# Performance work log

Hardware: AMD Instinct MI355X
Metric: run time of the kernel (lower is better)

The kernel has to match this reference:

```python
import jax, jax.numpy as jnp
import numpy as np
from jax import lax

DN = ('NHWC', 'HWIO', 'NHWC')
N_MEM = 2000  # memory slots
BN_EPS = 1e-3


def _conv(x, w, b):
    # tf.nn.conv2d stride 2, SAME, NHWC / HWIO
    return lax.conv_general_dilated(x, w, (2, 2), 'SAME', dimension_numbers=DN) + b


def _convt(x, w, b):
    # tf.nn.conv2d_transpose; w is TF layout [kh, kw, out_ch, in_ch]
    return lax.conv_transpose(x, w, (2, 2), 'SAME', dimension_numbers=DN,
                              transpose_kernel=True) + b


def _bn(x, g, b):
    # BatchNormalization(training=True): batch statistics over N,H,W
    m = jnp.mean(x, axis=(0, 1, 2))
    v = jnp.var(x, axis=(0, 1, 2))
    return g * (x - m) * lax.rsqrt(v + BN_EPS) + b


def setup_inputs() -> dict:
    key = jax.random.key(0)
    ks = iter(jax.random.split(key, 40))
    def gn(shape, s=0.05):
        return jax.random.normal(next(ks), shape, jnp.float32) * s
    inp = {'x': jax.random.uniform(next(ks), (16, 256, 256, 3), jnp.float32)}
    inp.update(
        w_e1=gn((1, 1, 3, 16)), b_e1=gn((16,)),
        g_bn1=jnp.ones(16, jnp.float32), be_bn1=jnp.zeros(16, jnp.float32),
        w_e2=gn((3, 3, 16, 32)), b_e2=gn((32,)),
        g_bn2=jnp.ones(32, jnp.float32), be_bn2=jnp.zeros(32, jnp.float32),
        w_e3=gn((3, 3, 32, 64)), b_e3=gn((64,)),
        g_bn3=jnp.ones(64, jnp.float32), be_bn3=jnp.zeros(64, jnp.float32),
        w_mem=gn((1, 1, N_MEM, 64)),
        w_d1=gn((3, 3, 32, 64)), b_d1=gn((32,)),
        g_bnt1=jnp.ones(32, jnp.float32), be_bnt1=jnp.zeros(32, jnp.float32),
        w_d2=gn((3, 3, 16, 32)), b_d2=gn((16,)),
        g_bnt2=jnp.ones(16, jnp.float32), be_bnt2=jnp.zeros(16, jnp.float32),
        w_d3=gn((3, 3, 3, 16)), b_d3=gn((3,)),
    )
    return inp


def reference(x, w_e1, b_e1, g_bn1, be_bn1, w_e2, b_e2, g_bn2, be_bn2,
              w_e3, b_e3, g_bn3, be_bn3, w_mem,
              w_d1, b_d1, g_bnt1, be_bnt1, w_d2, b_d2, g_bnt2, be_bnt2,
              w_d3, b_d3):
    # ---- encode ----
    h = jax.nn.relu(_bn(_conv(x, w_e1, b_e1), g_bn1, be_bn1))   # [B,128,128,16]
    h = jax.nn.relu(_bn(_conv(h, w_e2, b_e2), g_bn2, be_bn2))   # [B,64,64,32]
    z = jax.nn.relu(_bn(_conv(h, w_e3, b_e3), g_bn3, be_bn3))   # [B,32,32,64]
    # ---- memory addressing ----
    mem = w_mem[0, 0]                                            # [N, 64]
    num = jnp.einsum('bhwc,nc->bhwn', z, mem)
    den = jnp.einsum('bhwc,nc->bhwn', z * z, mem * mem)
    att = jax.nn.softmax((num + 1e-12) / (den + 1e-12), axis=-1)  # [B,32,32,N]
    d = att - 1.0 / N_MEM                                        # hard shrinkage
    renorm = jnp.clip(jax.nn.relu(d) * att / (jnp.abs(d) + 1e-12),
                      1e-12, 1.0 - 1e-12)
    z_hat = jnp.einsum('bhwn,nc->bhwc', renorm, mem)             # [B,32,32,64]
    # ---- decode ----
    t = jax.nn.relu(_bn(_convt(z_hat, w_d1, b_d1), g_bnt1, be_bnt1))  # [B,64,64,32]
    t = jax.nn.relu(_bn(_convt(t, w_d2, b_d2), g_bnt2, be_bnt2))      # [B,128,128,16]
    x_hat = jnp.clip(_convt(t, w_d3, b_d3), 1e-12, 1.0 - 1e-12)       # [B,256,256,3]
    return x_hat
```

## Files before the change

kernel.cpp:

```cpp
#include <hip/hip_runtime.h>
#include <math.h>

typedef __bf16 bf16x8 __attribute__((ext_vector_type(8)));
typedef __bf16 bf16x4 __attribute__((ext_vector_type(4)));
typedef float  f32x16 __attribute__((ext_vector_type(16)));

static __device__ __forceinline__ f32x16 zero16() {
  f32x16 v;
  #pragma unroll
  for (int i = 0; i < 16; ++i) v[i] = 0.f;
  return v;
}
static __device__ __forceinline__ unsigned int bfbits(__bf16 b) {
  return (unsigned int)__builtin_bit_cast(unsigned short, b);
}
static __device__ __forceinline__ bf16x8 mk8(unsigned int a, unsigned int b,
                                             unsigned int c, unsigned int d) {
  uint4 t; t.x = a; t.y = b; t.z = c; t.w = d;
  return __builtin_bit_cast(bf16x8, t);
}

__global__ __launch_bounds__(256) void k_conv1(const float* __restrict__ x,
    const float* __restrict__ w, const float* __restrict__ b, float* __restrict__ y,
    float* __restrict__ partials) {
  int t = blockIdx.x*256 + threadIdx.x;
  int ox = t & 127, oy = (t >> 7) & 127, bb = t >> 14;
  const float* xp = x + ((size_t)((bb*256 + 2*oy)*256 + 2*ox))*3;
  float x0 = xp[0], x1 = xp[1], x2 = xp[2];
  float4 rg[4];
  float4* yp = (float4*)(y + (size_t)t*16);
  #pragma unroll
  for (int g = 0; g < 4; ++g) {
    float4 r;
    r.x = b[g*4+0] + x0*w[g*4+0] + x1*w[16+g*4+0] + x2*w[32+g*4+0];
    r.y = b[g*4+1] + x0*w[g*4+1] + x1*w[16+g*4+1] + x2*w[32+g*4+1];
    r.z = b[g*4+2] + x0*w[g*4+2] + x1*w[16+g*4+2] + x2*w[32+g*4+2];
    r.w = b[g*4+3] + x0*w[g*4+3] + x1*w[16+g*4+3] + x2*w[32+g*4+3];
    rg[g] = r;
    yp[g] = r;
  }
  float4 s4[4], q4[4];
  #pragma unroll
  for (int g=0; g<4; ++g) {
    s4[g] = rg[g];
    q4[g] = make_float4(rg[g].x*rg[g].x, rg[g].y*rg[g].y, rg[g].z*rg[g].z, rg[g].w*rg[g].w);
  }
  #pragma unroll
  for (int off=1; off<64; off<<=1) {
    #pragma unroll
    for (int g=0; g<4; ++g) {
      s4[g].x += __shfl_xor(s4[g].x, off); s4[g].y += __shfl_xor(s4[g].y, off);
      s4[g].z += __shfl_xor(s4[g].z, off); s4[g].w += __shfl_xor(s4[g].w, off);
      q4[g].x += __shfl_xor(q4[g].x, off); q4[g].y += __shfl_xor(q4[g].y, off);
      q4[g].z += __shfl_xor(q4[g].z, off); q4[g].w += __shfl_xor(q4[g].w, off);
    }
  }
  __shared__ float red[4][32];
  int wv = threadIdx.x >> 6, lane = threadIdx.x & 63;
  if (lane == 0) {
    #pragma unroll
    for (int g=0; g<4; ++g) {
      *(float4*)&red[wv][g*4]      = s4[g];
      *(float4*)&red[wv][16 + g*4] = q4[g];
    }
  }
  __syncthreads();
  if (threadIdx.x < 32)
    partials[(size_t)blockIdx.x*32 + threadIdx.x] =
      red[0][threadIdx.x]+red[1][threadIdx.x]+red[2][threadIdx.x]+red[3][threadIdx.x];
}

template<int C,int CSPLIT>
__global__ __launch_bounds__(256) void k_finalize2(const float* __restrict__ partials, int nblk,
    double inv_n, const float* __restrict__ g, const float* __restrict__ be, float* __restrict__ ss) {
  const int COUTT = C/CSPLIT;
  const int NSTAT = 2*C;
  const int PER = 256/NSTAT;
  __shared__ double red[256];
  int tid = threadIdx.x;
  int st = tid % NSTAT, sub = tid / NSTAT;
  int c = st % C, kind = st / C;
  int cq = c / COUTT, j = c % COUTT;
  int nb = nblk / CSPLIT;
  double acc = 0.0;
  #pragma unroll 4
  for (int i = sub; i < nb; i += PER) {
    int bq = cq + i*CSPLIT;
    acc += (double)partials[(size_t)bq*2*COUTT + kind*COUTT + j];
  }
  red[tid] = acc;
  __syncthreads();
  for (int off = PER>>1; off > 0; off >>= 1) {
    if (sub < off) red[tid] += red[tid + off*NSTAT];
    __syncthreads();
  }
  if (tid < C) {
    double mean = red[tid]*inv_n;
    double var  = red[C+tid]*inv_n - mean*mean;
    float scale = g[tid] * rsqrtf((float)var + 1e-3f);
    float shift = be[tid] - (float)mean*scale;
    ss[tid] = scale; ss[C+tid] = shift;
  }
}

template<int CIN,int COUT,int CSPLIT,int HIN,int HOUT,bool BN>
__global__ __launch_bounds__(256) void k_conv_bn(const float* __restrict__ in,
    const float* __restrict__ w, const float* __restrict__ bias,
    const float* __restrict__ ss, float* __restrict__ y, float* __restrict__ partials) {
  const int COUTT = COUT/CSPLIT;
  const int NW4 = COUTT/4;
  __shared__ float4 wlds[9*CIN*NW4];
  int bid = blockIdx.x;
  int cq  = bid % CSPLIT;
  int pxb = bid / CSPLIT;
  int c0  = cq*COUTT;
  for (int e = threadIdx.x; e < 9*CIN*NW4; e += 256) {
    int r = e / NW4, cg = e % NW4;
    wlds[e] = *(const float4*)(w + (size_t)r*COUT + c0 + cg*4);
  }
  __syncthreads();
  int t0 = pxb*256 + threadIdx.x;
  float4 acc[NW4];
  #pragma unroll
  for (int g=0; g<NW4; ++g) acc[g] = *(const float4*)(bias + c0 + g*4);
  int ox = t0 % HOUT, oy = (t0/HOUT) % HOUT, bb = t0/(HOUT*HOUT);
  #pragma unroll 1
  for (int dy=0; dy<3; ++dy) {
    #pragma unroll 1
    for (int dx=0; dx<3; ++dx) {
      int tap = dy*3+dx;
      int iy = 2*oy + dy, ix = 2*ox + dx;
      if (iy < HIN && ix < HIN) {
        const float* bp = in + ((size_t)(bb*HIN + iy)*HIN + ix)*CIN;
        #pragma unroll
        for (int ci4=0; ci4<CIN/4; ++ci4) {
          float4 v = *(const float4*)(bp + ci4*4);
          if (BN) {
            float4 sc = *(const float4*)(ss + ci4*4);
            float4 sh = *(const float4*)(ss + CIN + ci4*4);
            v.x = fmaxf(0.f, fmaf(v.x, sc.x, sh.x));
            v.y = fmaxf(0.f, fmaf(v.y, sc.y, sh.y));
            v.z = fmaxf(0.f, fmaf(v.z, sc.z, sh.z));
            v.w = fmaxf(0.f, fmaf(v.w, sc.w, sh.w));
          }
          float va[4] = {v.x, v.y, v.z, v.w};
          #pragma unroll
          for (int k=0;k<4;++k) {
            float vk = va[k];
            #pragma unroll
            for (int g=0; g<NW4; ++g) {
              float4 w4 = wlds[(tap*CIN + ci4*4 + k)*NW4 + g];
              acc[g].x = fmaf(vk, w4.x, acc[g].x);
              acc[g].y = fmaf(vk, w4.y, acc[g].y);
              acc[g].z = fmaf(vk, w4.z, acc[g].z);
              acc[g].w = fmaf(vk, w4.w, acc[g].w);
            }
          }
        }
      }
    }
  }
  float4* yp = (float4*)(y + (size_t)t0*COUT + c0);
  #pragma unroll
  for (int g=0;g<NW4;++g) yp[g] = acc[g];
  float4 s4[NW4], q4[NW4];
  #pragma unroll
  for (int g=0; g<NW4; ++g) {
    s4[g] = acc[g];
    q4[g] = make_float4(acc[g].x*acc[g].x, acc[g].y*acc[g].y,
                        acc[g].z*acc[g].z, acc[g].w*acc[g].w);
  }
  #pragma unroll
  for (int off=1; off<64; off<<=1) {
    #pragma unroll
    for (int g=0; g<NW4; ++g) {
      s4[g].x += __shfl_xor(s4[g].x, off); s4[g].y += __shfl_xor(s4[g].y, off);
      s4[g].z += __shfl_xor(s4[g].z, off); s4[g].w += __shfl_xor(s4[g].w, off);
      q4[g].x += __shfl_xor(q4[g].x, off); q4[g].y += __shfl_xor(q4[g].y, off);
      q4[g].z += __shfl_xor(q4[g].z, off); q4[g].w += __shfl_xor(q4[g].w, off);
    }
  }
  __shared__ float red[4][2*COUTT];
  int wv = threadIdx.x >> 6, lane = threadIdx.x & 63;
  if (lane == 0) {
    #pragma unroll
    for (int g=0; g<NW4; ++g) {
      *(float4*)&red[wv][g*4]         = s4[g];
      *(float4*)&red[wv][COUTT + g*4] = q4[g];
    }
  }
  __syncthreads();
  if (threadIdx.x < 2*COUTT)
    partials[(size_t)bid*2*COUTT + threadIdx.x] =
      red[0][threadIdx.x]+red[1][threadIdx.x]+red[2][threadIdx.x]+red[3][threadIdx.x];
}


__global__ __launch_bounds__(256) void k_prep_z(const float* __restrict__ y3,
    const float* __restrict__ ss,
    __bf16* __restrict__ ZH, __bf16* __restrict__ ZL,
    __bf16* __restrict__ Z2H, __bf16* __restrict__ Z2L) {
  int t = blockIdx.x*256 + threadIdx.x;
  float4 v = ((const float4*)y3)[t];
  int c0 = (t*4) & 63;
  float4 sc = *(const float4*)(ss + c0);
  float4 sh = *(const float4*)(ss + 64 + c0);
  float vv[4];
  vv[0] = fmaxf(0.f, fmaf(v.x, sc.x, sh.x));
  vv[1] = fmaxf(0.f, fmaf(v.y, sc.y, sh.y));
  vv[2] = fmaxf(0.f, fmaf(v.z, sc.z, sh.z));
  vv[3] = fmaxf(0.f, fmaf(v.w, sc.w, sh.w));
  bf16x4 h, l, h2, l2;
  #pragma unroll
  for (int i=0;i<4;++i) {
    float f = vv[i];
    __bf16 hb = (__bf16)f;
    h[i] = hb; l[i] = (__bf16)(f - (float)hb);
    float q = f*f;
    __bf16 qb = (__bf16)q;
    h2[i] = qb; l2[i] = (__bf16)(q - (float)qb);
  }
  ((bf16x4*)ZH)[t] = h;  ((bf16x4*)ZL)[t] = l;
  ((bf16x4*)Z2H)[t] = h2; ((bf16x4*)Z2L)[t] = l2;
}

__global__ __launch_bounds__(256) void k_prep_m(const float* __restrict__ mem,
    __bf16* __restrict__ MH, __bf16* __restrict__ ML,
    __bf16* __restrict__ M2H, __bf16* __restrict__ M2L,
    __bf16* __restrict__ MHT, __bf16* __restrict__ MLT) {
  int t = blockIdx.x*256 + threadIdx.x;
  int n = t >> 4, c0 = (t & 15)*4;
  float4 v = make_float4(0.f,0.f,0.f,0.f);
  if (n < 2000) v = *(const float4*)(mem + (size_t)n*64 + c0);
  float vv[4] = {v.x, v.y, v.z, v.w};
  bf16x4 h, l, h2, l2;
  #pragma unroll
  for (int i=0;i<4;++i) {
    float f = vv[i];
    __bf16 hb = (__bf16)f;
    h[i] = hb; l[i] = (__bf16)(f - (float)hb);
    float q = f*f;
    __bf16 qb = (__bf16)q;
    h2[i] = qb; l2[i] = (__bf16)(q - (float)qb);
  }
  *(bf16x4*)(MH  + (size_t)n*64 + c0) = h;
  *(bf16x4*)(ML  + (size_t)n*64 + c0) = l;
  *(bf16x4*)(M2H + (size_t)n*64 + c0) = h2;
  *(bf16x4*)(M2L + (size_t)n*64 + c0) = l2;
  #pragma unroll
  for (int i=0;i<4;++i) {
    MHT[(size_t)(c0+i)*2048 + n] = h[i];
    MLT[(size_t)(c0+i)*2048 + n] = l[i];
  }
}

__global__ __launch_bounds__(256) void k_pass1(
    const __bf16* __restrict__ ZH, const __bf16* __restrict__ ZL,
    const __bf16* __restrict__ Z2H, const __bf16* __restrict__ Z2L,
    const __bf16* __restrict__ MH, const __bf16* __restrict__ ML,
    const __bf16* __restrict__ M2H, const __bf16* __restrict__ M2L,
    float* __restrict__ partM, float* __restrict__ partS) {
  int pb = blockIdx.x & 127, chunk = blockIdx.x >> 7;
  int wave = threadIdx.x >> 6, lane = threadIdx.x & 63;
  int p0 = pb*128 + wave*32;
  int col = lane & 31, hi = lane >> 5;
  bf16x8 bzh[4], bzl[4], b2h[4], b2l[4];
  size_t zoff = (size_t)(p0 + col)*64 + hi*8;
  #pragma unroll
  for (int ks=0;ks<4;++ks) {
    bzh[ks] = *(const bf16x8*)(ZH  + zoff + ks*16);
    bzl[ks] = *(const bf16x8*)(ZL  + zoff + ks*16);
    b2h[ks] = *(const bf16x8*)(Z2H + zoff + ks*16);
    b2l[ks] = *(const bf16x8*)(Z2L + zoff + ks*16);
  }
  float m = -3.4e38f, S = 0.f;
  int nbase = chunk*256;
  #pragma unroll 2
  for (int t=0; t<8; ++t) {
    int n0 = nbase + t*32;
    size_t arow = (size_t)(n0 + col)*64 + hi*8;
    f32x16 num = zero16(), den = zero16();
    #pragma unroll
    for (int ks=0;ks<4;++ks) {
      bf16x8 amh = *(const bf16x8*)(MH + arow + ks*16);
      bf16x8 aml = *(const bf16x8*)(ML + arow + ks*16);
      num = __builtin_amdgcn_mfma_f32_32x32x16_bf16(amh, bzh[ks], num, 0,0,0);
      num = __builtin_amdgcn_mfma_f32_32x32x16_bf16(amh, bzl[ks], num, 0,0,0);
      num = __builtin_amdgcn_mfma_f32_32x32x16_bf16(aml, bzh[ks], num, 0,0,0);
      bf16x8 a2h = *(const bf16x8*)(M2H + arow + ks*16);
      bf16x8 a2l = *(const bf16x8*)(M2L + arow + ks*16);
      den = __builtin_amdgcn_mfma_f32_32x32x16_bf16(a2h, b2h[ks], den, 0,0,0);
      den = __builtin_amdgcn_mfma_f32_32x32x16_bf16(a2h, b2l[ks], den, 0,0,0);
      den = __builtin_amdgcn_mfma_f32_32x32x16_bf16(a2l, b2h[ks], den, 0,0,0);
    }
    bool maskt = (n0 + 32 > 2000);
    float sv[16];
    float tmax = -3.4e38f;
    #pragma unroll
    for (int r=0;r<16;++r) {
      float s = (num[r] + 1e-12f) * __builtin_amdgcn_rcpf(den[r] + 1e-12f);
      if (maskt) {
        int nn = n0 + (r&3) + 8*(r>>2) + 4*hi;
        if (nn >= 2000) s = -3.4e38f;
      }
      sv[r] = s;
      tmax = fmaxf(tmax, s);
    }
    float mn = fmaxf(m, tmax);
    float ssum = 0.f;
    #pragma unroll
    for (int r=0;r<16;++r) ssum += __expf(sv[r] - mn);
    S = S*__expf(m - mn) + ssum;
    m = mn;
  }
  float mo = __shfl_xor(m, 32);
  float So = __shfl_xor(S, 32);
  float mf = fmaxf(m, mo);
  float Sf = S*__expf(m - mf) + So*__expf(mo - mf);
  if (lane < 32) {
    int p = p0 + col;
    partM[chunk*16384 + p] = mf;
    partS[chunk*16384 + p] = Sf;
  }
}

__global__ __launch_bounds__(256) void k_pass2(
    const __bf16* __restrict__ ZH, const __bf16* __restrict__ ZL,
    const __bf16* __restrict__ Z2H, const __bf16* __restrict__ Z2L,
    const __bf16* __restrict__ MH, const __bf16* __restrict__ ML,
    const __bf16* __restrict__ M2H, const __bf16* __restrict__ M2L,
    const __bf16* __restrict__ MHT, const __bf16* __restrict__ MLT,
    const float* __restrict__ partM, const float* __restrict__ partS,
    float* __restrict__ ZP) {
  int pb = blockIdx.x & 127, chunk = blockIdx.x >> 7;
  int wave = threadIdx.x >> 6, lane = threadIdx.x & 63;
  int p0 = pb*128 + wave*32;
  int col = lane & 31, hi = lane >> 5;
  bf16x8 bzh[4], bzl[4], b2h[4], b2l[4];
  size_t zoff = (size_t)(p0 + col)*64 + hi*8;
  #pragma unroll
  for (int ks=0;ks<4;++ks) {
    bzh[ks] = *(const bf16x8*)(ZH  + zoff + ks*16);
    bzl[ks] = *(const bf16x8*)(ZL  + zoff + ks*16);
    b2h[ks] = *(const bf16x8*)(Z2H + zoff + ks*16);
    b2l[ks] = *(const bf16x8*)(Z2L + zoff + ks*16);
  }
  int p = p0 + col;
  float pmv[8];
  float Mp = -3.4e38f;
  #pragma unroll
  for (int c=0;c<8;++c) { pmv[c] = partM[c*16384 + p]; Mp = fmaxf(Mp, pmv[c]); }
  float Ssum = 0.f;
  #pragma unroll
  for (int c=0;c<8;++c) Ssum += partS[c*16384 + p] * __expf(pmv[c] - Mp);
  float CM  = Mp + __logf(Ssum);
  float thr = CM - 7.6009025f;
  f32x16 za0 = zero16(), za1 = zero16();
  int nbase = chunk*256;
  #pragma unroll 2
  for (int t=0; t<8; ++t) {
    int n0 = nbase + t*32;
    size_t arow = (size_t)(n0 + col)*64 + hi*8;
    f32x16 num = zero16(), den = zero16();
    #pragma unroll
    for (int ks=0;ks<4;++ks) {
      bf16x8 amh = *(const bf16x8*)(MH + arow + ks*16);
      bf16x8 aml = *(const bf16x8*)(ML + arow + ks*16);
      num = __builtin_amdgcn_mfma_f32_32x32x16_bf16(amh, bzh[ks], num, 0,0,0);
      num = __builtin_amdgcn_mfma_f32_32x32x16_bf16(amh, bzl[ks], num, 0,0,0);
      num = __builtin_amdgcn_mfma_f32_32x32x16_bf16(aml, bzh[ks], num, 0,0,0);
      bf16x8 a2h = *(const bf16x8*)(M2H + arow + ks*16);
      bf16x8 a2l = *(const bf16x8*)(M2L + arow + ks*16);
      den = __builtin_amdgcn_mfma_f32_32x32x16_bf16(a2h, b2h[ks], den, 0,0,0);
      den = __builtin_amdgcn_mfma_f32_32x32x16_bf16(a2h, b2l[ks], den, 0,0,0);
      den = __builtin_amdgcn_mfma_f32_32x32x16_bf16(a2l, b2h[ks], den, 0,0,0);
    }
    bool maskt = (n0 + 32 > 2000);
    float rv[16];
    #pragma unroll
    for (int r=0;r<16;++r) {
      float s = (num[r] + 1e-12f) * __builtin_amdgcn_rcpf(den[r] + 1e-12f);
      float att = __expf(s - CM);
      float rr = (s > thr) ? att : 0.f;
      if (maskt) {
        int nn = n0 + (r&3) + 8*(r>>2) + 4*hi;
        if (nn >= 2000) rr = 0.f;
      }
      rv[r] = rr;
    }
    unsigned int qh[8];
    #pragma unroll
    for (int qd=0; qd<4; ++qd) {
      #pragma unroll
      for (int pr=0; pr<2; ++pr) {
        float r0 = rv[qd*4 + pr*2], r1 = rv[qd*4 + pr*2 + 1];
        qh[qd*2+pr] = bfbits((__bf16)r0) | (bfbits((__bf16)r1) << 16);
      }
    }
    unsigned int qhp[8];
    #pragma unroll
    for (int i=0;i<8;++i) qhp[i] = (unsigned int)__shfl_xor((int)qh[i], 32);
    bf16x8 f1h = hi ? mk8(qhp[2],qhp[3],qh[2],qh[3]) : mk8(qh[0],qh[1],qhp[0],qhp[1]);
    bf16x8 f2h = hi ? mk8(qhp[6],qhp[7],qh[6],qh[7]) : mk8(qh[4],qh[5],qhp[4],qhp[5]);
    #pragma unroll
    for (int kh=0; kh<2; ++kh) {
      bf16x8 fh = kh ? f2h : f1h;
      size_t bofs = (size_t)col*2048 + n0 + kh*16 + hi*8;
      bf16x8 bmh0 = *(const bf16x8*)(MHT + bofs);
      bf16x8 bml0 = *(const bf16x8*)(MLT + bofs);
      bf16x8 bmh1 = *(const bf16x8*)(MHT + bofs + (size_t)32*2048);
      bf16x8 bml1 = *(const bf16x8*)(MLT + bofs + (size_t)32*2048);
      za0 = __builtin_amdgcn_mfma_f32_32x32x16_bf16(fh, bmh0, za0, 0,0,0);
      za0 = __builtin_amdgcn_mfma_f32_32x32x16_bf16(fh, bml0, za0, 0,0,0);
      za1 = __builtin_amdgcn_mfma_f32_32x32x16_bf16(fh, bmh1, za1, 0,0,0);
      za1 = __builtin_amdgcn_mfma_f32_32x32x16_bf16(fh, bml1, za1, 0,0,0);
    }
  }
  size_t base = (size_t)chunk << 20;
  #pragma unroll
  for (int r=0;r<16;++r) {
    int prow = (r&3) + 8*(r>>2) + 4*hi;
    size_t o = base + (size_t)(p0 + prow)*64 + col;
    ZP[o]      = za0[r];
    ZP[o + 32] = za1[r];
  }
}

__global__ __launch_bounds__(256) void k_zcomb(const float* __restrict__ ZP,
                                               float* __restrict__ Gz) {
  int t = blockIdx.x*256 + threadIdx.x;
  float a = 0.f;
  #pragma unroll
  for (int c=0;c<8;++c) a += ZP[(size_t)c*1048576 + t];
  Gz[t] = a;
}

template<int CIN,int COUT,int CSPLIT,int HIN,bool BN>
__global__ __launch_bounds__(256) void k_convt_bn(const float* __restrict__ in,
    const float* __restrict__ w, const float* __restrict__ bias,
    const float* __restrict__ ss, float* __restrict__ y, float* __restrict__ partials) {
  const int COUTT = COUT/CSPLIT;
  const int HOUT = 2*HIN;
  __shared__ float4 wlds[4*COUTT*(CIN/4)];
  int bid = blockIdx.x;
  int cq = bid % CSPLIT; int rest = bid / CSPLIT;
  int cls = rest % 4;    int pxb = rest / 4;
  int pm = cls >> 1, pn = cls & 1;
  int c0 = cq*COUTT;
  int NTI = (pm == 0) ? 2 : 1;
  int NTJ = (pn == 0) ? 2 : 1;
  int NT = NTI*NTJ;
  for (int e = threadIdx.x; e < NT*COUTT*(CIN/4); e += 256) {
    int tl = e / (COUTT*(CIN/4));
    int rem = e % (COUTT*(CIN/4));
    int cc = rem / (CIN/4), ci4 = rem % (CIN/4);
    int ki = pm + 2*(tl / NTJ), kj = pn + 2*(tl % NTJ);
    wlds[e] = *(const float4*)(w + ((size_t)(ki*3+kj)*COUT + c0 + cc)*CIN + ci4*4);
  }
  __syncthreads();
  int t0 = pxb*256 + threadIdx.x;
  float acc[COUTT];
  #pragma unroll
  for (int cc=0;cc<COUTT;++cc) acc[cc] = bias[c0+cc];
  int nx = t0 % HIN, my = (t0/HIN) % HIN, bb = t0/(HIN*HIN);
  #pragma unroll 1
  for (int ti=0; ti<NTI; ++ti) {
    #pragma unroll 1
    for (int tj=0; tj<NTJ; ++tj) {
      int tl = ti*NTJ + tj;
      int i = my - ti, j = nx - tj;
      if (i >= 0 && j >= 0) {
        const float* bp = in + ((size_t)(bb*HIN + i)*HIN + j)*CIN;
        #pragma unroll
        for (int ci4=0; ci4<CIN/4; ++ci4) {
          float4 v = *(const float4*)(bp + ci4*4);
          if (BN) {
            float4 sc = *(const float4*)(ss + ci4*4);
            float4 sh = *(const float4*)(ss + CIN + ci4*4);
            v.x = fmaxf(0.f, fmaf(v.x, sc.x, sh.x));
            v.y = fmaxf(0.f, fmaf(v.y, sc.y, sh.y));
            v.z = fmaxf(0.f, fmaf(v.z, sc.z, sh.z));
            v.w = fmaxf(0.f, fmaf(v.w, sc.w, sh.w));
          }
          #pragma unroll
          for (int cc=0;cc<COUTT;++cc) {
            float4 w4 = wlds[(tl*COUTT + cc)*(CIN/4) + ci4];
            float a = acc[cc];
            a = fmaf(v.x, w4.x, a);
            a = fmaf(v.y, w4.y, a);
            a = fmaf(v.z, w4.z, a);
            a = fmaf(v.w, w4.w, a);
            acc[cc] = a;
          }
        }
      }
    }
  }
  int m = 2*my + pm, n = 2*nx + pn;
  float* yp = y + ((size_t)(bb*HOUT + m)*HOUT + n)*COUT + c0;
  #pragma unroll
  for (int g=0;g<COUTT/4;++g)
    ((float4*)yp)[g] = make_float4(acc[g*4], acc[g*4+1], acc[g*4+2], acc[g*4+3]);
  float s[COUTT], q[COUTT];
  #pragma unroll
  for (int cc=0;cc<COUTT;++cc) { s[cc] = acc[cc]; q[cc] = acc[cc]*acc[cc]; }
  #pragma unroll
  for (int off=1; off<64; off<<=1) {
    #pragma unroll
    for (int cc=0;cc<COUTT;++cc) {
      s[cc] += __shfl_xor(s[cc], off);
      q[cc] += __shfl_xor(q[cc], off);
    }
  }
  __shared__ float red[4][2*COUTT];
  int wv = threadIdx.x >> 6, lane = threadIdx.x & 63;
  if (lane == 0) {
    #pragma unroll
    for (int cc=0;cc<COUTT;++cc) { red[wv][cc] = s[cc]; red[wv][COUTT+cc] = q[cc]; }
  }
  __syncthreads();
  if (threadIdx.x < 2*COUTT)
    partials[(size_t)bid*2*COUTT + threadIdx.x] =
      red[0][threadIdx.x]+red[1][threadIdx.x]+red[2][threadIdx.x]+red[3][threadIdx.x];
}

__global__ __launch_bounds__(256) void k_convt_final(const float* __restrict__ in,
    const float* __restrict__ w, const float* __restrict__ bias,
    const float* __restrict__ ss, float* __restrict__ out) {
  const int CIN=16, HIN=128, HOUT=256;
  __shared__ float4 wlds[4*3*4];
  int cls = blockIdx.x & 3;
  int pxb = blockIdx.x >> 2;
  int pm = cls >> 1, pn = cls & 1;
  int NTI = (pm == 0) ? 2 : 1;
  int NTJ = (pn == 0) ? 2 : 1;
  int NT = NTI*NTJ;
  if (threadIdx.x < NT*3*4) {
    int e = threadIdx.x;
    int tl = e / 12, rem = e % 12;
    int c = rem / 4, ci4 = rem % 4;
    int ki = pm + 2*(tl / NTJ), kj = pn + 2*(tl % NTJ);
    wlds[e] = *(const float4*)(w + ((size_t)(ki*3+kj)*3 + c)*CIN + ci4*4);
  }
  __syncthreads();
  int t = pxb*256 + threadIdx.x;
  int nx = t % HIN, my = (t/HIN) % HIN, bb = t/(HIN*HIN);
  float a0 = bias[0], a1 = bias[1], a2 = bias[2];
  #pragma unroll 1
  for (int ti=0; ti<NTI; ++ti) {
    #pragma unroll 1
    for (int tj=0; tj<NTJ; ++tj) {
      int tl = ti*NTJ + tj;
      int i = my - ti, j = nx - tj;
      if (i >= 0 && j >= 0) {
        const float* bp = in + ((size_t)(bb*HIN + i)*HIN + j)*CIN;
        #pragma unroll
        for (int ci4=0; ci4<4; ++ci4) {
          float4 v = *(const float4*)(bp + ci4*4);
          float4 sc = *(const float4*)(ss + ci4*4);
          float4 sh = *(const float4*)(ss + CIN + ci4*4);
          v.x = fmaxf(0.f, fmaf(v.x, sc.x, sh.x));
          v.y = fmaxf(0.f, fmaf(v.y, sc.y, sh.y));
          v.z = fmaxf(0.f, fmaf(v.z, sc.z, sh.z));
          v.w = fmaxf(0.f, fmaf(v.w, sc.w, sh.w));
          float4 w0 = wlds[(tl*3 + 0)*4 + ci4];
          float4 w1 = wlds[(tl*3 + 1)*4 + ci4];
          float4 w2 = wlds[(tl*3 + 2)*4 + ci4];
          a0 = fmaf(v.x, w0.x, a0); a0 = fmaf(v.y, w0.y, a0);
          a0 = fmaf(v.z, w0.z, a0); a0 = fmaf(v.w, w0.w, a0);
          a1 = fmaf(v.x, w1.x, a1); a1 = fmaf(v.y, w1.y, a1);
          a1 = fmaf(v.z, w1.z, a1); a1 = fmaf(v.w, w1.w, a1);
          a2 = fmaf(v.x, w2.x, a2); a2 = fmaf(v.y, w2.y, a2);
          a2 = fmaf(v.z, w2.z, a2); a2 = fmaf(v.w, w2.w, a2);
        }
      }
    }
  }
  int m = 2*my + pm, n = 2*nx + pn;
  float* op = out + ((size_t)(bb*HOUT + m)*HOUT + n)*3;
  op[0] = fminf(fmaxf(a0, 1e-12f), 1.0f);
  op[1] = fminf(fmaxf(a1, 1e-12f), 1.0f);
  op[2] = fminf(fmaxf(a2, 1e-12f), 1.0f);
}

extern "C" void kernel_launch(void* const* d_in, const int* in_sizes, int n_in,
                              void* d_out, int out_size, void* d_ws, size_t ws_size,
                              hipStream_t stream) {
  const float* x    = (const float*)d_in[0];
  const float* w_e1 = (const float*)d_in[1];
  const float* b_e1 = (const float*)d_in[2];
  const float* g1   = (const float*)d_in[3];
  const float* be1  = (const float*)d_in[4];
  const float* w_e2 = (const float*)d_in[5];
  const float* b_e2 = (const float*)d_in[6];
  const float* g2   = (const float*)d_in[7];
  const float* be2  = (const float*)d_in[8];
  const float* w_e3 = (const float*)d_in[9];
  const float* b_e3 = (const float*)d_in[10];
  const float* g3   = (const float*)d_in[11];
  const float* be3  = (const float*)d_in[12];
  const float* wmem = (const float*)d_in[13];
  const float* w_d1 = (const float*)d_in[14];
  const float* b_d1 = (const float*)d_in[15];
  const float* gt1  = (const float*)d_in[16];
  const float* bet1 = (const float*)d_in[17];
  const float* w_d2 = (const float*)d_in[18];
  const float* b_d2 = (const float*)d_in[19];
  const float* gt2  = (const float*)d_in[20];
  const float* bet2 = (const float*)d_in[21];
  const float* w_d3 = (const float*)d_in[22];
  const float* b_d3 = (const float*)d_in[23];
  float* out = (float*)d_out;

  float* ws = (float*)d_ws;
  float* A  = ws;
  float* Cc = A  + 4194304;
  float* E  = Cc + 2097152;
  float* Gz = E  + 1048576;
  float* ZP = Gz + 1048576;
  float* bfbase = ZP + 8388608;
  __bf16* ZH  = (__bf16*)bfbase;
  __bf16* ZL  = ZH  + 16384*64;
  __bf16* Z2H = ZL  + 16384*64;
  __bf16* Z2L = Z2H + 16384*64;
  __bf16* MH  = Z2L + 16384*64;
  __bf16* ML  = MH  + 2048*64;
  __bf16* M2H = ML  + 2048*64;
  __bf16* M2L = M2H + 2048*64;
  __bf16* MHT = M2L + 2048*64;
  __bf16* MLT = MHT + 64*2048;
  float* PT   = (float*)(MLT + 64*2048);
  float* SS   = PT + 131072;
  float* PM   = SS + 256;
  float* PS   = PM + 131072;
  (void)ws_size; (void)in_sizes; (void)n_in; (void)out_size;

  k_conv1<<<1024,256,0,stream>>>(x, w_e1, b_e1, A, PT);
  k_finalize2<16,1><<<1,256,0,stream>>>(PT, 1024, 1.0/262144.0, g1, be1, SS);
  k_conv_bn<16,32,2,128,64,true><<<512,256,0,stream>>>(A, w_e2, b_e2, SS, Cc, PT);
  k_finalize2<32,2><<<1,256,0,stream>>>(PT, 512, 1.0/65536.0, g2, be2, SS);
  k_conv_bn<32,64,8,64,32,true><<<512,256,0,stream>>>(Cc, w_e3, b_e3, SS, E, PT);
  k_finalize2<64,8><<<1,256,0,stream>>>(PT, 512, 1.0/16384.0, g3, be3, SS);
  k_prep_m<<<128,256,0,stream>>>(wmem, MH, ML, M2H, M2L, MHT, MLT);
  k_prep_z<<<1024,256,0,stream>>>(E, SS, ZH, ZL, Z2H, Z2L);
  k_pass1<<<1024,256,0,stream>>>(ZH, ZL, Z2H, Z2L, MH, ML, M2H, M2L, PM, PS);
  k_pass2<<<1024,256,0,stream>>>(ZH, ZL, Z2H, Z2L, MH, ML, M2H, M2L, MHT, MLT, PM, PS, ZP);
  k_zcomb<<<4096,256,0,stream>>>(ZP, Gz);
  k_convt_bn<64,32,2,32,false><<<512,256,0,stream>>>(Gz, w_d1, b_d1, nullptr, Cc, PT);
  k_finalize2<32,2><<<1,256,0,stream>>>(PT, 512, 1.0/65536.0, gt1, bet1, SS);
  k_convt_bn<32,16,1,64,true><<<1024,256,0,stream>>>(Cc, w_d2, b_d2, SS, A, PT);
  k_finalize2<16,1><<<1,256,0,stream>>>(PT, 1024, 1.0/262144.0, gt2, bet2, SS);
  k_convt_final<<<4096,256,0,stream>>>(A, w_d3, b_d3, SS, out);
}
```

Baseline: 400.9 us.

## Switch memory-attention passes to 16x16x32 MFMA tiles with smaller per-wave blocks

Rewrites both memory-addressing passes to use 16x16x32 bf16 MFMA instead of 32x32x16. Each wave now handles 16 positions instead of 32, and the grid doubles to 2048 blocks. The softmax max/sum reduction now runs over four lane groups, and pass2 rebuilds the A fragment for the second GEMM with lane shuffles. Occupancy hints are added to the launch bounds. The intent is fewer accumulator registers and higher occupancy for better latency hiding, at the cost of more memory-row reloads per position and more shuffle work.

Result: slower. 582.7 us (+45.4%).

```diff
diff --git a/kernel.cpp b/kernel.cpp
--- a/kernel.cpp
+++ b/kernel.cpp
@@ -3,12 +3,10 @@
 
 typedef __bf16 bf16x8 __attribute__((ext_vector_type(8)));
 typedef __bf16 bf16x4 __attribute__((ext_vector_type(4)));
-typedef float  f32x16 __attribute__((ext_vector_type(16)));
-
-static __device__ __forceinline__ f32x16 zero16() {
-  f32x16 v;
-  #pragma unroll
-  for (int i = 0; i < 16; ++i) v[i] = 0.f;
+typedef float  f32x4  __attribute__((ext_vector_type(4)));
+
+static __device__ __forceinline__ f32x4 zero4() {
+  f32x4 v; v[0]=0.f; v[1]=0.f; v[2]=0.f; v[3]=0.f;
   return v;
 }
 static __device__ __forceinline__ unsigned int bfbits(__bf16 b) {
@@ -254,77 +252,78 @@
   }
 }
 
-__global__ __launch_bounds__(256) void k_pass1(
+__global__ __launch_bounds__(256,4) void k_pass1(
     const __bf16* __restrict__ ZH, const __bf16* __restrict__ ZL,
     const __bf16* __restrict__ Z2H, const __bf16* __restrict__ Z2L,
     const __bf16* __restrict__ MH, const __bf16* __restrict__ ML,
     const __bf16* __restrict__ M2H, const __bf16* __restrict__ M2L,
     float* __restrict__ partM, float* __restrict__ partS) {
-  int pb = blockIdx.x & 127, chunk = blockIdx.x >> 7;
+  int pb = blockIdx.x & 255, chunk = blockIdx.x >> 8;
   int wave = threadIdx.x >> 6, lane = threadIdx.x & 63;
-  int p0 = pb*128 + wave*32;
-  int col = lane & 31, hi = lane >> 5;
-  bf16x8 bzh[4], bzl[4], b2h[4], b2l[4];
-  size_t zoff = (size_t)(p0 + col)*64 + hi*8;
-  #pragma unroll
-  for (int ks=0;ks<4;++ks) {
-    bzh[ks] = *(const bf16x8*)(ZH  + zoff + ks*16);
-    bzl[ks] = *(const bf16x8*)(ZL  + zoff + ks*16);
-    b2h[ks] = *(const bf16x8*)(Z2H + zoff + ks*16);
-    b2l[ks] = *(const bf16x8*)(Z2L + zoff + ks*16);
+  int p0 = pb*64 + wave*16;
+  int pcol = lane & 15, g = (lane >> 4) & 3;
+  bf16x8 bzh[2], bzl[2], b2h[2], b2l[2];
+  size_t zoff = (size_t)(p0 + pcol)*64 + g*8;
+  #pragma unroll
+  for (int ks=0;ks<2;++ks) {
+    bzh[ks] = *(const bf16x8*)(ZH  + zoff + ks*32);
+    bzl[ks] = *(const bf16x8*)(ZL  + zoff + ks*32);
+    b2h[ks] = *(const bf16x8*)(Z2H + zoff + ks*32);
+    b2l[ks] = *(const bf16x8*)(Z2L + zoff + ks*32);
   }
   float m = -3.4e38f, S = 0.f;
   int nbase = chunk*256;
-  #pragma unroll 2
-  for (int t=0; t<8; ++t) {
-    int n0 = nbase + t*32;
-    size_t arow = (size_t)(n0 + col)*64 + hi*8;
-    f32x16 num = zero16(), den = zero16();
-    #pragma unroll
-    for (int ks=0;ks<4;++ks) {
-      bf16x8 amh = *(const bf16x8*)(MH + arow + ks*16);
-      bf16x8 aml = *(const bf16x8*)(ML + arow + ks*16);
-      num = __builtin_amdgcn_mfma_f32_32x32x16_bf16(amh, bzh[ks], num, 0,0,0);
-      num = __builtin_amdgcn_mfma_f32_32x32x16_bf16(amh, bzl[ks], num, 0,0,0);
-      num = __builtin_amdgcn_mfma_f32_32x32x16_bf16(aml, bzh[ks], num, 0,0,0);
-      bf16x8 a2h = *(const bf16x8*)(M2H + arow + ks*16);
-      bf16x8 a2l = *(const bf16x8*)(M2L + arow + ks*16);
-      den = __builtin_amdgcn_mfma_f32_32x32x16_bf16(a2h, b2h[ks], den, 0,0,0);
-      den = __builtin_amdgcn_mfma_f32_32x32x16_bf16(a2h, b2l[ks], den, 0,0,0);
-      den = __builtin_amdgcn_mfma_f32_32x32x16_bf16(a2l, b2h[ks], den, 0,0,0);
-    }
-    bool maskt = (n0 + 32 > 2000);
-    float sv[16];
+  #pragma unroll 4
+  for (int t=0; t<16; ++t) {
+    int n0 = nbase + t*16;
+    size_t arow = (size_t)(n0 + pcol)*64 + g*8;
+    f32x4 num = zero4(), den = zero4();
+    #pragma unroll
+    for (int ks=0;ks<2;++ks) {
+      bf16x8 amh = *(const bf16x8*)(MH + arow + ks*32);
+      bf16x8 aml = *(const bf16x8*)(ML + arow + ks*32);
+      num = __builtin_amdgcn_mfma_f32_16x16x32_bf16(amh, bzh[ks], num, 0,0,0);
+      num = __builtin_amdgcn_mfma_f32_16x16x32_bf16(amh, bzl[ks], num, 0,0,0);
+      num = __builtin_amdgcn_mfma_f32_16x16x32_bf16(aml, bzh[ks], num, 0,0,0);
+      bf16x8 a2h = *(const bf16x8*)(M2H + arow + ks*32);
+      bf16x8 a2l = *(const bf16x8*)(M2L + arow + ks*32);
+      den = __builtin_amdgcn_mfma_f32_16x16x32_bf16(a2h, b2h[ks], den, 0,0,0);
+      den = __builtin_amdgcn_mfma_f32_16x16x32_bf16(a2h, b2l[ks], den, 0,0,0);
+      den = __builtin_amdgcn_mfma_f32_16x16x32_bf16(a2l, b2h[ks], den, 0,0,0);
+    }
+    bool maskt = (n0 + 16 > 2000);
+    float sv[4];
     float tmax = -3.4e38f;
     #pragma unroll
-    for (int r=0;r<16;++r) {
-      float s = (num[r] + 1e-12f) * __builtin_amdgcn_rcpf(den[r] + 1e-12f);
-      if (maskt) {
-        int nn = n0 + (r&3) + 8*(r>>2) + 4*hi;
-        if (nn >= 2000) s = -3.4e38f;
-      }
-      sv[r] = s;
+    for (int i=0;i<4;++i) {
+      float s = (num[i] + 1e-12f) * __builtin_amdgcn_rcpf(den[i] + 1e-12f);
+      if (maskt && (n0 + 4*g + i >= 2000)) s = -3.4e38f;
+      sv[i] = s;
       tmax = fmaxf(tmax, s);
     }
     float mn = fmaxf(m, tmax);
     float ssum = 0.f;
     #pragma unroll
-    for (int r=0;r<16;++r) ssum += __expf(sv[r] - mn);
+    for (int i=0;i<4;++i) ssum += __expf(sv[i] - mn);
     S = S*__expf(m - mn) + ssum;
     m = mn;
   }
-  float mo = __shfl_xor(m, 32);
-  float So = __shfl_xor(S, 32);
-  float mf = fmaxf(m, mo);
-  float Sf = S*__expf(m - mf) + So*__expf(mo - mf);
-  if (lane < 32) {
-    int p = p0 + col;
-    partM[chunk*16384 + p] = mf;
-    partS[chunk*16384 + p] = Sf;
-  }
-}
-
-__global__ __launch_bounds__(256) void k_pass2(
+  #pragma unroll
+  for (int off=16; off<64; off<<=1) {
+    float mo = __shfl_xor(m, off);
+    float So = __shfl_xor(S, off);
+    float mf = fmaxf(m, mo);
+    S = S*__expf(m - mf) + So*__expf(mo - mf);
+    m = mf;
+  }
+  if (lane < 16) {
+    int p = p0 + lane;
+    partM[chunk*16384 + p] = m;
+    partS[chunk*16384 + p] = S;
+  }
+}
+
+__global__ __launch_bounds__(256,3) void k_pass2(
     const __bf16* __restrict__ ZH, const __bf16* __restrict__ ZL,
     const __bf16* __restrict__ Z2H, const __bf16* __restrict__ Z2L,
     const __bf16* __restrict__ MH, const __bf16* __restrict__ ML,
@@ -332,20 +331,20 @@
     const __bf16* __restrict__ MHT, const __bf16* __restrict__ MLT,
     const float* __restrict__ partM, const float* __restrict__ partS,
     float* __restrict__ ZP) {
-  int pb = blockIdx.x & 127, chunk = blockIdx.x >> 7;
+  int pb = blockIdx.x & 255, chunk = blockIdx.x >> 8;
   int wave = threadIdx.x >> 6, lane = threadIdx.x & 63;
-  int p0 = pb*128 + wave*32;
-  int col = lane & 31, hi = lane >> 5;
-  bf16x8 bzh[4], bzl[4], b2h[4], b2l[4];
-  size_t zoff = (size_t)(p0 + col)*64 + hi*8;
-  #pragma unroll
-  for (int ks=0;ks<4;++ks) {
-    bzh[ks] = *(const bf16x8*)(ZH  + zoff + ks*16);
-    bzl[ks] = *(const bf16x8*)(ZL  + zoff + ks*16);
-    b2h[ks] = *(const bf16x8*)(Z2H + zoff + ks*16);
-    b2l[ks] = *(const bf16x8*)(Z2L + zoff + ks*16);
-  }
-  int p = p0 + col;
+  int p0 = pb*64 + wave*16;
+  int pcol = lane & 15, g = (lane >> 4) & 3;
+  bf16x8 bzh[2], bzl[2], b2h[2], b2l[2];
+  size_t zoff = (size_t)(p0 + pcol)*64 + g*8;
+  #pragma unroll
+  for (int ks=0;ks<2;++ks) {
+    bzh[ks] = *(const bf16x8*)(ZH  + zoff + ks*32);
+    bzl[ks] = *(const bf16x8*)(ZL  + zoff + ks*32);
+    b2h[ks] = *(const bf16x8*)(Z2H + zoff + ks*32);
+    b2l[ks] = *(const bf16x8*)(Z2L + zoff + ks*32);
+  }
+  int p = p0 + pcol;
   float pmv[8];
   float Mp = -3.4e38f;
   #pragma unroll
@@ -355,74 +354,92 @@
   for (int c=0;c<8;++c) Ssum += partS[c*16384 + p] * __expf(pmv[c] - Mp);
   float CM  = Mp + __logf(Ssum);
   float thr = CM - 7.6009025f;
-  f32x16 za0 = zero16(), za1 = zero16();
+  f32x4 za0 = zero4(), za1 = zero4(), za2 = zero4(), za3 = zero4();
   int nbase = chunk*256;
+  int sA = pcol + ((g & 1) ? 32 : 0);
+  int sB = sA + 16;
+  bool th = (g >= 2);
   #pragma unroll 2
   for (int t=0; t<8; ++t) {
     int n0 = nbase + t*32;
-    size_t arow = (size_t)(n0 + col)*64 + hi*8;
-    f32x16 num = zero16(), den = zero16();
-    #pragma unroll
-    for (int ks=0;ks<4;++ks) {
-      bf16x8 amh = *(const bf16x8*)(MH + arow + ks*16);
-      bf16x8 aml = *(const bf16x8*)(ML + arow + ks*16);
-      num = __builtin_amdgcn_mfma_f32_32x32x16_bf16(amh, bzh[ks], num, 0,0,0);
-      num = __builtin_amdgcn_mfma_f32_32x32x16_bf16(amh, bzl[ks], num, 0,0,0);
-      num = __builtin_amdgcn_mfma_f32_32x32x16_bf16(aml, bzh[ks], num, 0,0,0);
-      bf16x8 a2h = *(const bf16x8*)(M2H + arow + ks*16);
-      bf16x8 a2l = *(const bf16x8*)(M2L + arow + ks*16);
-      den = __builtin_amdgcn_mfma_f32_32x32x16_bf16(a2h, b2h[ks], den, 0,0,0);
-      den = __builtin_amdgcn_mfma_f32_32x32x16_bf16(a2h, b2l[ks], den, 0,0,0);
-      den = __builtin_amdgcn_mfma_f32_32x32x16_bf16(a2l, b2h[ks], den, 0,0,0);
-    }
-    bool maskt = (n0 + 32 > 2000);
-    float rv[16];
-    #pragma unroll
-    for (int r=0;r<16;++r) {
-      float s = (num[r] + 1e-12f) * __builtin_amdgcn_rcpf(den[r] + 1e-12f);
-      float att = __expf(s - CM);
-      float rr = (s > thr) ? att : 0.f;
-      if (maskt) {
-        int nn = n0 + (r&3) + 8*(r>>2) + 4*hi;
-        if (nn >= 2000) rr = 0.f;
+    unsigned int q00, q01, q10, q11;
+    #pragma unroll
+    for (int st=0; st<2; ++st) {
+      int nt0 = n0 + st*16;
+      size_t arow = (size_t)(nt0 + pcol)*64 + g*8;
+      f32x4 num = zero4(), den = zero4();
+      #pragma unroll
+      for (int ks=0;ks<2;++ks) {
+        bf16x8 amh = *(const bf16x8*)(MH + arow + ks*32);
+        bf16x8 aml = *(const bf16x8*)(ML + arow + ks*32);
+        num = __builtin_amdgcn_mfma_f32_16x16x32_bf16(amh, bzh[ks], num, 0,0,0);
+        num = __builtin_amdgcn_mfma_f32_16x16x32_bf16(amh, bzl[ks], num, 0,0,0);
+        num = __builtin_amdgcn_mfma_f32_16x16x32_bf16(aml, bzh[ks], num, 0,0,0);
+        bf16x8 a2h = *(const bf16x8*)(M2H + arow + ks*32);
+        bf16x8 a2l = *(const bf16x8*)(M2L + arow + ks*32);
+        den = __builtin_amdgcn_mfma_f32_16x16x32_bf16(a2h, b2h[ks], den, 0,0,0);
+        den = __builtin_amdgcn_mfma_f32_16x16x32_bf16(a2h, b2l[ks], den, 0,0,0);
+        den = __builtin_amdgcn_mfma_f32_16x16x32_bf16(a2l, b2h[ks], den, 0,0,0);
       }
-      rv[r] = rr;
-    }
-    unsigned int qh[8];
-    #pragma unroll
-    for (int qd=0; qd<4; ++qd) {
+      bool maskt = (nt0 + 16 > 2000);
+      float rv[4];
       #pragma unroll
-      for (int pr=0; pr<2; ++pr) {
-        float r0 = rv[qd*4 + pr*2], r1 = rv[qd*4 + pr*2 + 1];
-        qh[qd*2+pr] = bfbits((__bf16)r0) | (bfbits((__bf16)r1) << 16);
+      for (int i=0;i<4;++i) {
+        float s = (num[i] + 1e-12f) * __builtin_amdgcn_rcpf(den[i] + 1e-12f);
+        float att = __expf(s - CM);
+        float rr = (s > thr) ? att : 0.f;
+        if (maskt && (nt0 + 4*g + i >= 2000)) rr = 0.f;
+        rv[i] = rr;
       }
-    }
-    unsigned int qhp[8];
-    #pragma unroll
-    for (int i=0;i<8;++i) qhp[i] = (unsigned int)__shfl_xor((int)qh[i], 32);
-    bf16x8 f1h = hi ? mk8(qhp[2],qhp[3],qh[2],qh[3]) : mk8(qh[0],qh[1],qhp[0],qhp[1]);
-    bf16x8 f2h = hi ? mk8(qhp[6],qhp[7],qh[6],qh[7]) : mk8(qh[4],qh[5],qhp[4],qhp[5]);
-    #pragma unroll
-    for (int kh=0; kh<2; ++kh) {
-      bf16x8 fh = kh ? f2h : f1h;
-      size_t bofs = (size_t)col*2048 + n0 + kh*16 + hi*8;
-      bf16x8 bmh0 = *(const bf16x8*)(MHT + bofs);
-      bf16x8 bml0 = *(const bf16x8*)(MLT + bofs);
-      bf16x8 bmh1 = *(const bf16x8*)(MHT + bofs + (size_t)32*2048);
-      bf16x8 bml1 = *(const bf16x8*)(MLT + bofs + (size_t)32*2048);
-      za0 = __builtin_amdgcn_mfma_f32_32x32x16_bf16(fh, bmh0, za0, 0,0,0);
-      za0 = __builtin_amdgcn_mfma_f32_32x32x16_bf16(fh, bml0, za0, 0,0,0);
-      za1 = __builtin_amdgcn_mfma_f32_32x32x16_bf16(fh, bmh1, za1, 0,0,0);
-      za1 = __builtin_amdgcn_mfma_f32_32x32x16_bf16(fh, bml1, za1, 0,0,0);
-    }
-  }
-  size_t base = (size_t)chunk << 20;
-  #pragma unroll
-  for (int r=0;r<16;++r) {
-    int prow = (r&3) + 8*(r>>2) + 4*hi;
-    size_t o = base + (size_t)(p0 + prow)*64 + col;
-    ZP[o]      = za0[r];
-    ZP[o + 32] = za1[r];
+      unsigned int w0 = bfbits((__bf16)rv[0]) | (bfbits((__bf16)rv[1]) << 16);
+      unsigned int w1 = bfbits((__bf16)rv[2]) | (bfbits((__bf16)rv[3]) << 16);
+      if (st == 0) { q00 = w0; q01 = w1; } else { q10 = w0; q11 = w1; }
+    }
+    unsigned int x00 = (unsigned int)__shfl((int)q00, sA);
+    unsigned int x01 = (unsigned int)__shfl((int)q01, sA);
+    unsigned int x02 = (unsigned int)__shfl((int)q00, sB);
+    unsigned int x03 = (unsigned int)__shfl((int)q01, sB);
+    unsigned int x10 = (unsigned int)__shfl((int)q10, sA);
+    unsigned int x11 = (unsigned int)__shfl((int)q11, sA);
+    unsigned int x12 = (unsigned int)__shfl((int)q10, sB);
+    unsigned int x13 = (unsigned int)__shfl((int)q11, sB);
+    bf16x8 afrag = mk8(th?x10:x00, th?x11:x01, th?x12:x02, th?x13:x03);
+    {
+      size_t bofs = (size_t)(0*16 + pcol)*2048 + n0 + g*8;
+      bf16x8 bmh = *(const bf16x8*)(MHT + bofs);
+      bf16x8 bml = *(const bf16x8*)(MLT + bofs);
+      za0 = __builtin_amdgcn_mfma_f32_16x16x32_bf16(afrag, bmh, za0, 0,0,0);
+      za0 = __builtin_amdgcn_mfma_f32_16x16x32_bf16(afrag, bml, za0, 0,0,0);
+    }
+    {
+      size_t bofs = (size_t)(1*16 + pcol)*2048 + n0 + g*8;
+      bf16x8 bmh = *(const bf16x8*)(MHT + bofs);
+      bf16x8 bml = *(const bf16x8*)(MLT + bofs);
+      za1 = __builtin_amdgcn_mfma_f32_16x16x32_bf16(afrag, bmh, za1, 0,0,0);
+      za1 = __builtin_amdgcn_mfma_f32_16x16x32_bf16(afrag, bml, za1, 0,0,0);
+    }
+    {
+      size_t bofs = (size_t)(2*16 + pcol)*2048 + n0 + g*8;
+      bf16x8 bmh = *(const bf16x8*)(MHT + bofs);
+      bf16x8 bml = *(const bf16x8*)(MLT + bofs);
+      za2 = __builtin_amdgcn_mfma_f32_16x16x32_bf16(afrag, bmh, za2, 0,0,0);
+      za2 = __builtin_amdgcn_mfma_f32_16x16x32_bf16(afrag, bml, za2, 0,0,0);
+    }
+    {
+      size_t bofs = (size_t)(3*16 + pcol)*2048 + n0 + g*8;
+      bf16x8 bmh = *(const bf16x8*)(MHT + bofs);
+      bf16x8 bml = *(const bf16x8*)(MLT + bofs);
+      za3 = __builtin_amdgcn_mfma_f32_16x16x32_bf16(afrag, bmh, za3, 0,0,0);
+      za3 = __builtin_amdgcn_mfma_f32_16x16x32_bf16(afrag, bml, za3, 0,0,0);
+    }
+  }
+  size_t base = ((size_t)chunk << 20) + (size_t)(p0 + 4*g)*64 + pcol;
+  #pragma unroll
+  for (int i=0;i<4;++i) {
+    ZP[base + (size_t)i*64]      = za0[i];
+    ZP[base + (size_t)i*64 + 16] = za1[i];
+    ZP[base + (size_t)i*64 + 32] = za2[i];
+    ZP[base + (size_t)i*64 + 48] = za3[i];
   }
 }
 
@@ -643,8 +660,8 @@
   k_finalize2<64,8><<<1,256,0,stream>>>(PT, 512, 1.0/16384.0, g3, be3, SS);
   k_prep_m<<<128,256,0,stream>>>(wmem, MH, ML, M2H, M2L, MHT, MLT);
   k_prep_z<<<1024,256,0,stream>>>(E, SS, ZH, ZL, Z2H, Z2L);
-  k_pass1<<<1024,256,0,stream>>>(ZH, ZL, Z2H, Z2L, MH, ML, M2H, M2L, PM, PS);
-  k_pass2<<<1024,256,0,stream>>>(ZH, ZL, Z2H, Z2L, MH, ML, M2H, M2L, MHT, MLT, PM, PS, ZP);
+  k_pass1<<<2048,256,0,stream>>>(ZH, ZL, Z2H, Z2L, MH, ML, M2H, M2L, PM, PS);
+  k_pass2<<<2048,256,0,stream>>>(ZH, ZL, Z2H, Z2L, MH, ML, M2H, M2L, MHT, MLT, PM, PS, ZP);
   k_zcomb<<<4096,256,0,stream>>>(ZP, Gz);
   k_convt_bn<64,32,2,32,false><<<512,256,0,stream>>>(Gz, w_d1, b_d1, nullptr, Cc, PT);
   k_finalize2<32,2><<<1,256,0,stream>>>(PT, 512, 1.0/65536.0, gt1, bet1, SS);
```

## Store pass1 attention scores to workspace and reuse them in pass2

Applied to the files above, without the earlier changes.

Pass1 now writes the per-slot attention score (num/den) for every position to a large fp32 workspace buffer, and pass2 reads these scores instead of recomputing the split-bf16 MFMA products. This removes half of the memory-addressing matrix work and the Z/M operand loads from pass2. In exchange it adds a write and a read of a roughly 128 MB intermediate, and the workspace layout is rearranged so the buffer overlaps dead activation buffers.

Result: faster. 385.9 us (-3.7%).

```diff
diff --git a/kernel.cpp b/kernel.cpp
--- a/kernel.cpp
+++ b/kernel.cpp
@@ -259,7 +259,7 @@
     const __bf16* __restrict__ Z2H, const __bf16* __restrict__ Z2L,
     const __bf16* __restrict__ MH, const __bf16* __restrict__ ML,
     const __bf16* __restrict__ M2H, const __bf16* __restrict__ M2L,
-    float* __restrict__ partM, float* __restrict__ partS) {
+    float* __restrict__ S32, float* __restrict__ partM, float* __restrict__ partS) {
   int pb = blockIdx.x & 127, chunk = blockIdx.x >> 7;
   int wave = threadIdx.x >> 6, lane = threadIdx.x & 63;
   int p0 = pb*128 + wave*32;
@@ -306,6 +306,13 @@
       sv[r] = s;
       tmax = fmaxf(tmax, s);
     }
+    {
+      size_t sbase = ((size_t)((chunk*8 + t)*16384 + p0 + col)*2 + hi)*16;
+      *(float4*)(S32 + sbase)      = make_float4(sv[0], sv[1], sv[2], sv[3]);
+      *(float4*)(S32 + sbase + 4)  = make_float4(sv[4], sv[5], sv[6], sv[7]);
+      *(float4*)(S32 + sbase + 8)  = make_float4(sv[8], sv[9], sv[10], sv[11]);
+      *(float4*)(S32 + sbase + 12) = make_float4(sv[12], sv[13], sv[14], sv[15]);
+    }
     float mn = fmaxf(m, tmax);
     float ssum = 0.f;
     #pragma unroll
@@ -325,10 +332,7 @@
 }
 
 __global__ __launch_bounds__(256) void k_pass2(
-    const __bf16* __restrict__ ZH, const __bf16* __restrict__ ZL,
-    const __bf16* __restrict__ Z2H, const __bf16* __restrict__ Z2L,
-    const __bf16* __restrict__ MH, const __bf16* __restrict__ ML,
-    const __bf16* __restrict__ M2H, const __bf16* __restrict__ M2L,
+    const float* __restrict__ S32,
     const __bf16* __restrict__ MHT, const __bf16* __restrict__ MLT,
     const float* __restrict__ partM, const float* __restrict__ partS,
     float* __restrict__ ZP) {
@@ -336,15 +340,6 @@
   int wave = threadIdx.x >> 6, lane = threadIdx.x & 63;
   int p0 = pb*128 + wave*32;
   int col = lane & 31, hi = lane >> 5;
-  bf16x8 bzh[4], bzl[4], b2h[4], b2l[4];
-  size_t zoff = (size_t)(p0 + col)*64 + hi*8;
-  #pragma unroll
-  for (int ks=0;ks<4;++ks) {
-    bzh[ks] = *(const bf16x8*)(ZH  + zoff + ks*16);
-    bzl[ks] = *(const bf16x8*)(ZL  + zoff + ks*16);
-    b2h[ks] = *(const bf16x8*)(Z2H + zoff + ks*16);
-    b2l[ks] = *(const bf16x8*)(Z2L + zoff + ks*16);
-  }
   int p = p0 + col;
   float pmv[8];
   float Mp = -3.4e38f;
@@ -360,33 +355,19 @@
   #pragma unroll 2
   for (int t=0; t<8; ++t) {
     int n0 = nbase + t*32;
-    size_t arow = (size_t)(n0 + col)*64 + hi*8;
-    f32x16 num = zero16(), den = zero16();
-    #pragma unroll
-    for (int ks=0;ks<4;++ks) {
-      bf16x8 amh = *(const bf16x8*)(MH + arow + ks*16);
-      bf16x8 aml = *(const bf16x8*)(ML + arow + ks*16);
-      num = __builtin_amdgcn_mfma_f32_32x32x16_bf16(amh, bzh[ks], num, 0,0,0);
-      num = __builtin_amdgcn_mfma_f32_32x32x16_bf16(amh, bzl[ks], num, 0,0,0);
-      num = __builtin_amdgcn_mfma_f32_32x32x16_bf16(aml, bzh[ks], num, 0,0,0);
-      bf16x8 a2h = *(const bf16x8*)(M2H + arow + ks*16);
-      bf16x8 a2l = *(const bf16x8*)(M2L + arow + ks*16);
-      den = __builtin_amdgcn_mfma_f32_32x32x16_bf16(a2h, b2h[ks], den, 0,0,0);
-      den = __builtin_amdgcn_mfma_f32_32x32x16_bf16(a2h, b2l[ks], den, 0,0,0);
-      den = __builtin_amdgcn_mfma_f32_32x32x16_bf16(a2l, b2h[ks], den, 0,0,0);
-    }
-    bool maskt = (n0 + 32 > 2000);
+    size_t sbase = ((size_t)((chunk*8 + t)*16384 + p)*2 + hi)*16;
+    float4 sq0 = *(const float4*)(S32 + sbase);
+    float4 sq1 = *(const float4*)(S32 + sbase + 4);
+    float4 sq2 = *(const float4*)(S32 + sbase + 8);
+    float4 sq3 = *(const float4*)(S32 + sbase + 12);
+    float sv[16] = {sq0.x,sq0.y,sq0.z,sq0.w, sq1.x,sq1.y,sq1.z,sq1.w,
+                    sq2.x,sq2.y,sq2.z,sq2.w, sq3.x,sq3.y,sq3.z,sq3.w};
     float rv[16];
     #pragma unroll
     for (int r=0;r<16;++r) {
-      float s = (num[r] + 1e-12f) * __builtin_amdgcn_rcpf(den[r] + 1e-12f);
+      float s = sv[r];
       float att = __expf(s - CM);
-      float rr = (s > thr) ? att : 0.f;
-      if (maskt) {
-        int nn = n0 + (r&3) + 8*(r>>2) + 4*hi;
-        if (nn >= 2000) rr = 0.f;
-      }
-      rv[r] = rr;
+      rv[r] = (s > thr) ? att : 0.f;
     }
     unsigned int qh[8];
     #pragma unroll
@@ -613,12 +594,13 @@
   float* out = (float*)d_out;
 
   float* ws = (float*)d_ws;
-  float* A  = ws;
-  float* Cc = A  + 4194304;
-  float* E  = Cc + 2097152;
-  float* Gz = E  + 1048576;
-  float* ZP = Gz + 1048576;
-  float* bfbase = ZP + 8388608;
+  float* S32 = ws;
+  float* A   = ws;
+  float* Cc  = ws + 4194304;
+  float* Gz  = ws + 33554432;
+  float* ZP  = Gz + 1048576;
+  float* E   = ZP + 8388608;
+  float* bfbase = E + 1048576;
   __bf16* ZH  = (__bf16*)bfbase;
   __bf16* ZL  = ZH  + 16384*64;
   __bf16* Z2H = ZL  + 16384*64;
@@ -643,8 +625,8 @@
   k_finalize2<64,8><<<1,256,0,stream>>>(PT, 512, 1.0/16384.0, g3, be3, SS);
   k_prep_m<<<128,256,0,stream>>>(wmem, MH, ML, M2H, M2L, MHT, MLT);
   k_prep_z<<<1024,256,0,stream>>>(E, SS, ZH, ZL, Z2H, Z2L);
-  k_pass1<<<1024,256,0,stream>>>(ZH, ZL, Z2H, Z2L, MH, ML, M2H, M2L, PM, PS);
-  k_pass2<<<1024,256,0,stream>>>(ZH, ZL, Z2H, Z2L, MH, ML, M2H, M2L, MHT, MLT, PM, PS, ZP);
+  k_pass1<<<1024,256,0,stream>>>(ZH, ZL, Z2H, Z2L, MH, ML, M2H, M2L, S32, PM, PS);
+  k_pass2<<<1024,256,0,stream>>>(S32, MHT, MLT, PM, PS, ZP);
   k_zcomb<<<4096,256,0,stream>>>(ZP, Gz);
   k_convt_bn<64,32,2,32,false><<<512,256,0,stream>>>(Gz, w_d1, b_d1, nullptr, Cc, PT);
   k_finalize2<32,2><<<1,256,0,stream>>>(PT, 512, 1.0/65536.0, gt1, bet1, SS);
```
